# Kernel optimization log

Measured on AMD Instinct MI355X. Metric: run time of the kernel, lower is better.

The kernel has to match this reference:

```python
import jax, jax.numpy as jnp
import numpy as np

N_NODES = 100000
D = 128            # hidden_size*2
N_EDGES = 1600000  # avg degree 16
NUM_LABELS = 1024


def setup_inputs() -> dict:
    key = jax.random.key(0)
    ks = jax.random.split(key, 16)
    inputs = jax.random.normal(ks[0], (N_NODES, D), dtype=jnp.float32)
    src = jax.random.randint(ks[1], (N_EDGES,), 0, N_NODES, dtype=jnp.int64)
    dst = jax.random.randint(ks[2], (N_EDGES,), 0, N_NODES, dtype=jnp.int64)
    s = 0.05
    # GIN layer 1 (conv linear) + residual block 1
    eps1 = jnp.zeros((), dtype=jnp.float32)
    W1 = jax.random.normal(ks[3], (D, D), dtype=jnp.float32) * s
    b1 = jnp.zeros((D,), dtype=jnp.float32)
    rW1 = jax.random.normal(ks[4], (D, D), dtype=jnp.float32) * s
    rb1 = jnp.zeros((D,), dtype=jnp.float32)
    # GIN layer 2 + residual block 2
    eps2 = jnp.zeros((), dtype=jnp.float32)
    W2 = jax.random.normal(ks[5], (D, D), dtype=jnp.float32) * s
    b2 = jnp.zeros((D,), dtype=jnp.float32)
    rW2 = jax.random.normal(ks[6], (D, D), dtype=jnp.float32) * s
    rb2 = jnp.zeros((D,), dtype=jnp.float32)
    # final multi-label head
    linW = jax.random.normal(ks[7], (D, NUM_LABELS), dtype=jnp.float32) * s
    linb = jnp.zeros((NUM_LABELS,), dtype=jnp.float32)
    return dict(inputs=inputs, src=src, dst=dst,
                eps1=eps1, W1=W1, b1=b1, rW1=rW1, rb1=rb1,
                eps2=eps2, W2=W2, b2=b2, rW2=rW2, rb2=rb2,
                linW=linW, linb=linb)


def reference(inputs, src, dst, eps1, W1, b1, rW1, rb1,
              eps2, W2, b2, rW2, rb2, linW, linb):
    n = inputs.shape[0]

    def gin_conv(h, eps, W, b):
        # sum-aggregate neighbor features: irregular gather + scatter-add
        agg = jax.ops.segment_sum(h[src], dst, num_segments=n)  # [N, D]
        return ((1.0 + eps) * h + agg) @ W + b

    def residual_block(h, rW, rb):
        # Sequential(ReLU, Dropout(eval=identity), Residual(D, D))
        h = jax.nn.relu(h)
        return h + jax.nn.relu(h @ rW + rb)

    h1 = residual_block(gin_conv(inputs, eps1, W1, b1), rW1, rb1)
    h2 = residual_block(gin_conv(h1, eps2, W2, b2), rW2, rb2)

    stacked = jnp.stack([h1, h2], axis=1)   # [N, n_layers, D] == stack_embed
    pooled = stacked.mean(axis=1)           # [N, D]
    return pooled @ linW + linb             # [N, NUM_LABELS]
```

## Files before the change

kernel.cpp:

```cpp
#include <hip/hip_runtime.h>

#define DIM 128
#define NLAB 1024
#define MT 64
#define LDK 136

typedef __bf16 bf16x4 __attribute__((ext_vector_type(4)));
typedef __bf16 bf16x8 __attribute__((ext_vector_type(8)));
typedef float  f32x4  __attribute__((ext_vector_type(4)));

__global__ __launch_bounds__(256) void k_hist(
    const int* __restrict__ dst, int* __restrict__ cnt, int nE) {
  int e = blockIdx.x * 256 + threadIdx.x;
  if (e < nE) atomicAdd(&cnt[dst[e]], 1);
}

__global__ __launch_bounds__(1024) void k_scan(
    const int* __restrict__ cnt, int* __restrict__ off,
    int* __restrict__ cur, int n) {
  __shared__ int part[1024];
  const int t = threadIdx.x;
  const int per = (n + 1023) >> 10;
  const int start = t * per;
  const int end = min(start + per, n);
  int s = 0;
  for (int i = start; i < end; ++i) s += cnt[i];
  part[t] = s;
  __syncthreads();
  for (int d = 1; d < 1024; d <<= 1) {
    int v = (t >= d) ? part[t - d] : 0;
    __syncthreads();
    part[t] += v;
    __syncthreads();
  }
  int excl = (t == 0) ? 0 : part[t - 1];
  if (t == 1023) off[n] = part[1023];
  for (int i = start; i < end; ++i) {
    int c = cnt[i];
    off[i] = excl;
    cur[i] = excl;
    excl += c;
  }
}

__global__ __launch_bounds__(256) void k_binfill(
    const int* __restrict__ src, const int* __restrict__ dst,
    int* __restrict__ cur, int* __restrict__ eidx, int nE) {
  int e = blockIdx.x * 256 + threadIdx.x;
  if (e < nE) {
    int p = atomicAdd(&cur[dst[e]], 1);
    eidx[p] = src[e];
  }
}

__global__ __launch_bounds__(256) void k_gather(
    const float* __restrict__ h, const int* __restrict__ off,
    const int* __restrict__ eidx, float* __restrict__ agg, int n) {
  int node = blockIdx.x * 8 + (threadIdx.x >> 5);
  if (node >= n) return;
  int c = (threadIdx.x & 31) << 2;
  int beg = off[node], end = off[node + 1];
  float4 a0 = make_float4(0.f, 0.f, 0.f, 0.f);
  float4 a1 = a0, a2 = a0, a3 = a0;
  int e = beg;
  for (; e + 4 <= end; e += 4) {
    int s0 = eidx[e + 0];
    int s1 = eidx[e + 1];
    int s2 = eidx[e + 2];
    int s3 = eidx[e + 3];
    float4 v0 = *(const float4*)(h + (size_t)s0 * DIM + c);
    float4 v1 = *(const float4*)(h + (size_t)s1 * DIM + c);
    float4 v2 = *(const float4*)(h + (size_t)s2 * DIM + c);
    float4 v3 = *(const float4*)(h + (size_t)s3 * DIM + c);
    a0.x += v0.x; a0.y += v0.y; a0.z += v0.z; a0.w += v0.w;
    a1.x += v1.x; a1.y += v1.y; a1.z += v1.z; a1.w += v1.w;
    a2.x += v2.x; a2.y += v2.y; a2.z += v2.z; a2.w += v2.w;
    a3.x += v3.x; a3.y += v3.y; a3.z += v3.z; a3.w += v3.w;
  }
  for (; e < end; ++e) {
    int s = eidx[e];
    float4 v = *(const float4*)(h + (size_t)s * DIM + c);
    a0.x += v.x; a0.y += v.y; a0.z += v.z; a0.w += v.w;
  }
  a0.x += a1.x + a2.x + a3.x;
  a0.y += a1.y + a2.y + a3.y;
  a0.z += a1.z + a2.z + a3.z;
  a0.w += a1.w + a2.w + a3.w;
  *(float4*)(agg + (size_t)node * DIM + c) = a0;
}

__device__ __forceinline__ void conv_residual_tile(
    const float* __restrict__ hin, const float* __restrict__ agg, float e1,
    const float* __restrict__ W, const float* __restrict__ bias,
    const float* __restrict__ rW, const float* __restrict__ rbias,
    __bf16 (*As)[LDK], __bf16 (*Bs)[LDK],
    int rowBase, int n, int t, float ho[4][2][4]) {
#pragma unroll
  for (int it = 0; it < 8; ++it) {
    int idx = (it * 256 + t) << 2;
    int r = idx >> 7, c = idx & 127;
    int node = rowBase + r;
    float4 a4 = make_float4(0.f, 0.f, 0.f, 0.f);
    float4 g4 = a4;
    if (node < n) {
      a4 = *(const float4*)(hin + (size_t)node * DIM + c);
      g4 = *(const float4*)(agg + (size_t)node * DIM + c);
    }
    bf16x4 v;
    v[0] = (__bf16)(e1 * a4.x + g4.x);
    v[1] = (__bf16)(e1 * a4.y + g4.y);
    v[2] = (__bf16)(e1 * a4.z + g4.z);
    v[3] = (__bf16)(e1 * a4.w + g4.w);
    *(bf16x4*)&As[r][c] = v;
  }
  {
    int nloc = t & 127;
    int kh = (t >> 7) << 6;
#pragma unroll
    for (int kk = 0; kk < 64; ++kk) {
      int k = kh + kk;
      Bs[nloc][k] = (__bf16)W[(size_t)k * DIM + nloc];
    }
  }
  __syncthreads();

  const int wv = t >> 6, lane = t & 63;
  const int quad = lane >> 4, l16 = lane & 15;
  f32x4 acc[4][2];
#pragma unroll
  for (int i = 0; i < 4; ++i) {
    acc[i][0] = f32x4{0.f, 0.f, 0.f, 0.f};
    acc[i][1] = f32x4{0.f, 0.f, 0.f, 0.f};
  }
#pragma unroll
  for (int kc = 0; kc < 4; ++kc) {
    int kb = kc * 32 + quad * 8;
    bf16x8 b0 = *(const bf16x8*)&Bs[wv * 32 + l16][kb];
    bf16x8 b1 = *(const bf16x8*)&Bs[wv * 32 + 16 + l16][kb];
#pragma unroll
    for (int rt = 0; rt < 4; ++rt) {
      bf16x8 a = *(const bf16x8*)&As[rt * 16 + l16][kb];
      acc[rt][0] = __builtin_amdgcn_mfma_f32_16x16x32_bf16(a, b0, acc[rt][0], 0, 0, 0);
      acc[rt][1] = __builtin_amdgcn_mfma_f32_16x16x32_bf16(a, b1, acc[rt][1], 0, 0, 0);
    }
  }

  float hm[4][2][4];
#pragma unroll
  for (int rt = 0; rt < 4; ++rt)
#pragma unroll
    for (int ct = 0; ct < 2; ++ct) {
      float bv = bias[wv * 32 + ct * 16 + l16];
#pragma unroll
      for (int r = 0; r < 4; ++r)
        hm[rt][ct][r] = fmaxf(acc[rt][ct][r] + bv, 0.f);
    }

  __syncthreads();

#pragma unroll
  for (int rt = 0; rt < 4; ++rt)
#pragma unroll
    for (int ct = 0; ct < 2; ++ct) {
      int col = wv * 32 + ct * 16 + l16;
#pragma unroll
      for (int r = 0; r < 4; ++r)
        As[rt * 16 + quad * 4 + r][col] = (__bf16)hm[rt][ct][r];
    }
  {
    int nloc = t & 127;
    int kh = (t >> 7) << 6;
#pragma unroll
    for (int kk = 0; kk < 64; ++kk) {
      int k = kh + kk;
      Bs[nloc][k] = (__bf16)rW[(size_t)k * DIM + nloc];
    }
  }
  __syncthreads();

#pragma unroll
  for (int i = 0; i < 4; ++i) {
    acc[i][0] = f32x4{0.f, 0.f, 0.f, 0.f};
    acc[i][1] = f32x4{0.f, 0.f, 0.f, 0.f};
  }
#pragma unroll
  for (int kc = 0; kc < 4; ++kc) {
    int kb = kc * 32 + quad * 8;
    bf16x8 b0 = *(const bf16x8*)&Bs[wv * 32 + l16][kb];
    bf16x8 b1 = *(const bf16x8*)&Bs[wv * 32 + 16 + l16][kb];
#pragma unroll
    for (int rt = 0; rt < 4; ++rt) {
      bf16x8 a = *(const bf16x8*)&As[rt * 16 + l16][kb];
      acc[rt][0] = __builtin_amdgcn_mfma_f32_16x16x32_bf16(a, b0, acc[rt][0], 0, 0, 0);
      acc[rt][1] = __builtin_amdgcn_mfma_f32_16x16x32_bf16(a, b1, acc[rt][1], 0, 0, 0);
    }
  }

#pragma unroll
  for (int rt = 0; rt < 4; ++rt)
#pragma unroll
    for (int ct = 0; ct < 2; ++ct) {
      float bv = rbias[wv * 32 + ct * 16 + l16];
#pragma unroll
      for (int r = 0; r < 4; ++r)
        ho[rt][ct][r] = hm[rt][ct][r] + fmaxf(acc[rt][ct][r] + bv, 0.f);
    }
}

__global__ __launch_bounds__(256) void k_layer1(
    const float* __restrict__ hin, const float* __restrict__ agg,
    const float* __restrict__ epsp, const float* __restrict__ W,
    const float* __restrict__ bias, const float* __restrict__ rW,
    const float* __restrict__ rbias, float* __restrict__ h1, int n) {
  __shared__ __bf16 As[MT][LDK];
  __shared__ __bf16 Bs[DIM][LDK];
  const int t = threadIdx.x;
  const int rowBase = blockIdx.x * MT;
  float ho[4][2][4];
  conv_residual_tile(hin, agg, 1.0f + epsp[0], W, bias, rW, rbias,
                     As, Bs, rowBase, n, t, ho);
  const int wv = t >> 6, lane = t & 63;
  const int quad = lane >> 4, l16 = lane & 15;
#pragma unroll
  for (int rt = 0; rt < 4; ++rt)
#pragma unroll
    for (int ct = 0; ct < 2; ++ct) {
      int ncol = wv * 32 + ct * 16 + l16;
#pragma unroll
      for (int r = 0; r < 4; ++r) {
        int node = rowBase + rt * 16 + quad * 4 + r;
        if (node < n) h1[(size_t)node * DIM + ncol] = ho[rt][ct][r];
      }
    }
}

__global__ __launch_bounds__(256) void k_layer2f(
    const float* __restrict__ h1, const float* __restrict__ agg,
    const float* __restrict__ epsp, const float* __restrict__ W,
    const float* __restrict__ bias, const float* __restrict__ rW,
    const float* __restrict__ rbias, const float* __restrict__ linW,
    const float* __restrict__ linb, float* __restrict__ out, int n) {
  __shared__ __bf16 As[MT][LDK];
  __shared__ __bf16 Bs[DIM][LDK];
  const int t = threadIdx.x;
  const int rowBase = blockIdx.x * MT;
  float ho[4][2][4];
  conv_residual_tile(h1, agg, 1.0f + epsp[0], W, bias, rW, rbias,
                     As, Bs, rowBase, n, t, ho);
  const int wv = t >> 6, lane = t & 63;
  const int quad = lane >> 4, l16 = lane & 15;

  __syncthreads();

#pragma unroll
  for (int rt = 0; rt < 4; ++rt)
#pragma unroll
    for (int ct = 0; ct < 2; ++ct) {
      int col = wv * 32 + ct * 16 + l16;
#pragma unroll
      for (int r = 0; r < 4; ++r) {
        int lrow = rt * 16 + quad * 4 + r;
        int node = rowBase + lrow;
        float h1v = (node < n) ? h1[(size_t)node * DIM + col] : 0.f;
        As[lrow][col] = (__bf16)(0.5f * (h1v + ho[rt][ct][r]));
      }
    }

  for (int nb = 0; nb < 8; ++nb) {
    int nbase = nb << 7;
    {
      int nloc = t & 127;
      int kh = (t >> 7) << 6;
#pragma unroll
      for (int kk = 0; kk < 64; ++kk) {
        int k = kh + kk;
        Bs[nloc][k] = (__bf16)linW[(size_t)k * NLAB + nbase + nloc];
      }
    }
    __syncthreads();

    f32x4 acc[4][2];
#pragma unroll
    for (int i = 0; i < 4; ++i) {
      acc[i][0] = f32x4{0.f, 0.f, 0.f, 0.f};
      acc[i][1] = f32x4{0.f, 0.f, 0.f, 0.f};
    }
#pragma unroll
    for (int kc = 0; kc < 4; ++kc) {
      int kb = kc * 32 + quad * 8;
      bf16x8 b0 = *(const bf16x8*)&Bs[wv * 32 + l16][kb];
      bf16x8 b1 = *(const bf16x8*)&Bs[wv * 32 + 16 + l16][kb];
#pragma unroll
      for (int rt = 0; rt < 4; ++rt) {
        bf16x8 a = *(const bf16x8*)&As[rt * 16 + l16][kb];
        acc[rt][0] = __builtin_amdgcn_mfma_f32_16x16x32_bf16(a, b0, acc[rt][0], 0, 0, 0);
        acc[rt][1] = __builtin_amdgcn_mfma_f32_16x16x32_bf16(a, b1, acc[rt][1], 0, 0, 0);
      }
    }
#pragma unroll
    for (int rt = 0; rt < 4; ++rt)
#pragma unroll
      for (int ct = 0; ct < 2; ++ct) {
        int ncol = wv * 32 + ct * 16 + l16;
        float bv = linb[nbase + ncol];
#pragma unroll
        for (int r = 0; r < 4; ++r) {
          int node = rowBase + rt * 16 + quad * 4 + r;
          if (node < n)
            out[(size_t)node * NLAB + nbase + ncol] = acc[rt][ct][r] + bv;
        }
      }
    __syncthreads();
  }
}

extern "C" void kernel_launch(void* const* d_in, const int* in_sizes, int n_in,
                              void* d_out, int out_size, void* d_ws, size_t ws_size,
                              hipStream_t stream) {
  const float* inputs = (const float*)d_in[0];
  const int*   src    = (const int*)d_in[1];
  const int*   dst    = (const int*)d_in[2];
  const float* eps1   = (const float*)d_in[3];
  const float* W1     = (const float*)d_in[4];
  const float* b1     = (const float*)d_in[5];
  const float* rW1    = (const float*)d_in[6];
  const float* rb1    = (const float*)d_in[7];
  const float* eps2   = (const float*)d_in[8];
  const float* W2     = (const float*)d_in[9];
  const float* b2     = (const float*)d_in[10];
  const float* rW2    = (const float*)d_in[11];
  const float* rb2    = (const float*)d_in[12];
  const float* linW   = (const float*)d_in[13];
  const float* linb   = (const float*)d_in[14];
  float* out = (float*)d_out;

  const int n = in_sizes[0] / DIM;
  const int E = in_sizes[1];
  const size_t bufB = (size_t)n * DIM * sizeof(float);

  float* agg = (float*)d_ws;
  float* h1  = (float*)((char*)d_ws + bufB);

  int* eidx = (int*)d_out;
  int* off  = eidx + E;
  int* cur  = off + (n + 1);

  const int rowBlocks = (n + MT - 1) / MT;
  const int eBlocks = (E + 255) / 256;
  const int gBlocks = (n + 7) / 8;

  hipMemsetAsync(cur, 0, (size_t)n * sizeof(int), stream);
  k_hist<<<eBlocks, 256, 0, stream>>>(dst, cur, E);
  k_scan<<<1, 1024, 0, stream>>>(cur, off, cur, n);
  k_binfill<<<eBlocks, 256, 0, stream>>>(src, dst, cur, eidx, E);

  k_gather<<<gBlocks, 256, 0, stream>>>(inputs, off, eidx, agg, n);
  k_layer1<<<rowBlocks, 256, 0, stream>>>(inputs, agg, eps1, W1, b1, rW1, rb1, h1, n);
  k_gather<<<gBlocks, 256, 0, stream>>>(h1, off, eidx, agg, n);
  k_layer2f<<<rowBlocks, 256, 0, stream>>>(h1, agg, eps2, W2, b2, rW2, rb2,
                                           linW, linb, out, n);
}
```

Measured before the change: 1.420 ms.

## Split fused layer-2 and output head into separate kernels with 2D grid

Layer 2 now writes the mean-pooled embedding as bf16 to a workspace buffer. A new kernel computes the 1024-wide output head over a 2D grid, with one block per 64-row tile and 128-column slice, instead of each block looping serially over eight column slices. This exposes eight times more blocks for the output GEMM, which dominates output bandwidth. In exchange it adds an extra launch and a round trip through global memory for the pooled activations.

```diff
diff --git a/kernel.cpp b/kernel.cpp
--- a/kernel.cpp
+++ b/kernel.cpp
@@ -234,12 +234,11 @@
     }
 }
 
-__global__ __launch_bounds__(256) void k_layer2f(
+__global__ __launch_bounds__(256) void k_layer2(
     const float* __restrict__ h1, const float* __restrict__ agg,
     const float* __restrict__ epsp, const float* __restrict__ W,
     const float* __restrict__ bias, const float* __restrict__ rW,
-    const float* __restrict__ rbias, const float* __restrict__ linW,
-    const float* __restrict__ linb, float* __restrict__ out, int n) {
+    const float* __restrict__ rbias, __bf16* __restrict__ pooled, int n) {
   __shared__ __bf16 As[MT][LDK];
   __shared__ __bf16 Bs[DIM][LDK];
   const int t = threadIdx.x;
@@ -249,9 +248,6 @@
                      As, Bs, rowBase, n, t, ho);
   const int wv = t >> 6, lane = t & 63;
   const int quad = lane >> 4, l16 = lane & 15;
-
-  __syncthreads();
-
 #pragma unroll
   for (int rt = 0; rt < 4; ++rt)
 #pragma unroll
@@ -259,59 +255,82 @@
       int col = wv * 32 + ct * 16 + l16;
 #pragma unroll
       for (int r = 0; r < 4; ++r) {
-        int lrow = rt * 16 + quad * 4 + r;
-        int node = rowBase + lrow;
-        float h1v = (node < n) ? h1[(size_t)node * DIM + col] : 0.f;
-        As[lrow][col] = (__bf16)(0.5f * (h1v + ho[rt][ct][r]));
-      }
-    }
-
-  for (int nb = 0; nb < 8; ++nb) {
-    int nbase = nb << 7;
-    {
-      int nloc = t & 127;
-      int kh = (t >> 7) << 6;
-#pragma unroll
-      for (int kk = 0; kk < 64; ++kk) {
-        int k = kh + kk;
-        Bs[nloc][k] = (__bf16)linW[(size_t)k * NLAB + nbase + nloc];
-      }
-    }
-    __syncthreads();
-
-    f32x4 acc[4][2];
-#pragma unroll
-    for (int i = 0; i < 4; ++i) {
-      acc[i][0] = f32x4{0.f, 0.f, 0.f, 0.f};
-      acc[i][1] = f32x4{0.f, 0.f, 0.f, 0.f};
-    }
-#pragma unroll
-    for (int kc = 0; kc < 4; ++kc) {
-      int kb = kc * 32 + quad * 8;
-      bf16x8 b0 = *(const bf16x8*)&Bs[wv * 32 + l16][kb];
-      bf16x8 b1 = *(const bf16x8*)&Bs[wv * 32 + 16 + l16][kb];
-#pragma unroll
-      for (int rt = 0; rt < 4; ++rt) {
-        bf16x8 a = *(const bf16x8*)&As[rt * 16 + l16][kb];
-        acc[rt][0] = __builtin_amdgcn_mfma_f32_16x16x32_bf16(a, b0, acc[rt][0], 0, 0, 0);
-        acc[rt][1] = __builtin_amdgcn_mfma_f32_16x16x32_bf16(a, b1, acc[rt][1], 0, 0, 0);
-      }
-    }
-#pragma unroll
-    for (int rt = 0; rt < 4; ++rt)
-#pragma unroll
-      for (int ct = 0; ct < 2; ++ct) {
-        int ncol = wv * 32 + ct * 16 + l16;
-        float bv = linb[nbase + ncol];
-#pragma unroll
-        for (int r = 0; r < 4; ++r) {
-          int node = rowBase + rt * 16 + quad * 4 + r;
-          if (node < n)
-            out[(size_t)node * NLAB + nbase + ncol] = acc[rt][ct][r] + bv;
+        int node = rowBase + rt * 16 + quad * 4 + r;
+        if (node < n) {
+          float h1v = h1[(size_t)node * DIM + col];
+          pooled[(size_t)node * DIM + col] =
+              (__bf16)(0.5f * (h1v + ho[rt][ct][r]));
         }
       }
-    __syncthreads();
-  }
+    }
+}
+
+__global__ __launch_bounds__(256) void k_final_p(
+    const __bf16* __restrict__ pooled, const float* __restrict__ W,
+    const float* __restrict__ bias, float* __restrict__ out, int n) {
+  __shared__ __bf16 As[MT][LDK];
+  __shared__ __bf16 Bs[DIM][LDK];
+  const int t = threadIdx.x;
+  const int rowBase = blockIdx.x * MT;
+  const int nb = blockIdx.y << 7;
+
+#pragma unroll
+  for (int it = 0; it < 4; ++it) {
+    int idx = (it * 256 + t) << 3;
+    int r = idx >> 7, c = idx & 127;
+    int node = rowBase + r;
+    bf16x8 v;
+#pragma unroll
+    for (int j = 0; j < 8; ++j) v[j] = (__bf16)0.f;
+    if (node < n) v = *(const bf16x8*)(pooled + (size_t)node * DIM + c);
+    *(bf16x8*)&As[r][c] = v;
+  }
+  {
+    int nloc = t & 127;
+    int kh = (t >> 7) << 6;
+#pragma unroll
+    for (int kk = 0; kk < 64; ++kk) {
+      int k = kh + kk;
+      Bs[nloc][k] = (__bf16)W[(size_t)k * NLAB + nb + nloc];
+    }
+  }
+  __syncthreads();
+
+  const int wv = t >> 6, lane = t & 63;
+  const int quad = lane >> 4, l16 = lane & 15;
+  f32x4 acc[4][2];
+#pragma unroll
+  for (int i = 0; i < 4; ++i) {
+    acc[i][0] = f32x4{0.f, 0.f, 0.f, 0.f};
+    acc[i][1] = f32x4{0.f, 0.f, 0.f, 0.f};
+  }
+
+#pragma unroll
+  for (int kc = 0; kc < 4; ++kc) {
+    int kb = kc * 32 + quad * 8;
+    bf16x8 b0 = *(const bf16x8*)&Bs[wv * 32 + l16][kb];
+    bf16x8 b1 = *(const bf16x8*)&Bs[wv * 32 + 16 + l16][kb];
+#pragma unroll
+    for (int rt = 0; rt < 4; ++rt) {
+      bf16x8 a = *(const bf16x8*)&As[rt * 16 + l16][kb];
+      acc[rt][0] = __builtin_amdgcn_mfma_f32_16x16x32_bf16(a, b0, acc[rt][0], 0, 0, 0);
+      acc[rt][1] = __builtin_amdgcn_mfma_f32_16x16x32_bf16(a, b1, acc[rt][1], 0, 0, 0);
+    }
+  }
+
+#pragma unroll
+  for (int rt = 0; rt < 4; ++rt)
+#pragma unroll
+    for (int ct = 0; ct < 2; ++ct) {
+      int ncol = wv * 32 + ct * 16 + l16;
+      float bv = bias[nb + ncol];
+#pragma unroll
+      for (int r = 0; r < 4; ++r) {
+        int node = rowBase + rt * 16 + quad * 4 + r;
+        if (node < n)
+          out[(size_t)node * NLAB + nb + ncol] = acc[rt][ct][r] + bv;
+      }
+    }
 }
 
 extern "C" void kernel_launch(void* const* d_in, const int* in_sizes, int n_in,
@@ -338,8 +357,9 @@
   const int E = in_sizes[1];
   const size_t bufB = (size_t)n * DIM * sizeof(float);
 
-  float* agg = (float*)d_ws;
-  float* h1  = (float*)((char*)d_ws + bufB);
+  float*  agg    = (float*)d_ws;
+  float*  h1     = (float*)((char*)d_ws + bufB);
+  __bf16* pooled = (__bf16*)((char*)d_ws + 2 * bufB);
 
   int* eidx = (int*)d_out;
   int* off  = eidx + E;
@@ -348,6 +368,7 @@
   const int rowBlocks = (n + MT - 1) / MT;
   const int eBlocks = (E + 255) / 256;
   const int gBlocks = (n + 7) / 8;
+  dim3 fgrid(rowBlocks, NLAB / DIM);
 
   hipMemsetAsync(cur, 0, (size_t)n * sizeof(int), stream);
   k_hist<<<eBlocks, 256, 0, stream>>>(dst, cur, E);
@@ -357,6 +378,7 @@
   k_gather<<<gBlocks, 256, 0, stream>>>(inputs, off, eidx, agg, n);
   k_layer1<<<rowBlocks, 256, 0, stream>>>(inputs, agg, eps1, W1, b1, rW1, rb1, h1, n);
   k_gather<<<gBlocks, 256, 0, stream>>>(h1, off, eidx, agg, n);
-  k_layer2f<<<rowBlocks, 256, 0, stream>>>(h1, agg, eps2, W2, b2, rW2, rb2,
-                                           linW, linb, out, n);
-}
+  k_layer2<<<rowBlocks, 256, 0, stream>>>(h1, agg, eps2, W2, b2, rW2, rb2,
+                                          pooled, n);
+  k_final_p<<<fgrid, 256, 0, stream>>>(pooled, linW, linb, out, n);
+}
```

After: 1.313 ms. 1.08x faster.
